# Optimization experiments

Measured on AMD Instinct MI355X. Metric: run time of the kernel, lower is better.

Reference implementation:

```python
import jax, jax.numpy as jnp
import numpy as np
import math

B, T, N, D = 8, 12, 500, 512  # batch, time(heads), nodes, K*d
FACTOR = 5
SAMPLE_K = min(FACTOR * math.ceil(math.log(N)), N)  # = 35, also n_top (N_Q == N_K)
W_SCALE = 0.02


def setup_inputs() -> dict:
    key = jax.random.key(0)
    ks = jax.random.split(key, 9)
    f32 = jnp.float32
    return {
        "X":   jax.random.normal(ks[0], (B, T, N, D), f32),
        "STE": jax.random.normal(ks[1], (B, T, N, D), f32),
        "Wq":  jax.random.normal(ks[2], (2 * D, D), f32) * W_SCALE,
        "bq":  jnp.zeros((D,), f32),
        "Wk":  jax.random.normal(ks[3], (2 * D, D), f32) * W_SCALE,
        "bk":  jnp.zeros((D,), f32),
        "Wv":  jax.random.normal(ks[4], (2 * D, D), f32) * W_SCALE,
        "bv":  jnp.zeros((D,), f32),
        "sample_idx": jax.random.randint(ks[5], (N, SAMPLE_K), 0, N, jnp.int32),
    }


def reference(X, STE, Wq, bq, Wk, bk, Wv, bv, sample_idx):
    # concat spatial features with spatio-temporal embedding -> projections
    Xc = jnp.concatenate([X, STE], axis=-1)                  # [B,T,N,2D]
    q = jax.nn.relu(Xc @ Wq + bq)                            # [B,T,N,D]
    k = jax.nn.relu(Xc @ Wk + bk)
    v = jax.nn.relu(Xc @ Wv + bv)

    n_top = SAMPLE_K
    # _prob_QK: sampled Q-K scores. Since SAMPLE_K*D >> N, computing the full
    # [B,T,N,N] score matrix and gathering the sampled columns is strictly
    # cheaper in memory than materializing K_sample [B,T,N,S,D] as torch does;
    # the math (Q_K_sample values) is identical.
    scores_full = jnp.einsum('bhld,bhmd->bhlm', q, k)        # [B,T,N,N]
    QK_sample = jnp.take_along_axis(
        scores_full, sample_idx[None, None, :, :], axis=3)   # [B,T,N,S]
    # sparsity measure M = max - mean (mean over L_K = N)
    M = QK_sample.max(axis=-1) - QK_sample.sum(axis=-1) / N  # [B,T,N]
    _, idx = jax.lax.top_k(M, n_top)                         # [B,T,n_top]

    # reduced-query full attention scores (gather rows of full scores == Q_reduce @ K^T)
    scores = jnp.take_along_axis(scores_full, idx[..., None], axis=2)  # [B,T,u,N]
    scores = scores * (1.0 / math.sqrt(D))

    # ProbMask (mask_flag=True): causal mask per selected query position
    j = jnp.arange(N)
    mask = j[None, None, None, :] > idx[..., None]           # [B,T,u,N]
    scores = jnp.where(mask, -jnp.inf, scores)
    attn = jax.nn.softmax(scores, axis=-1)                   # [B,T,u,N]
    ctx_new = jnp.einsum('bhun,bhnd->bhud', attn, v)         # [B,T,u,D]

    # initial context = causal cumsum of V, then scatter-update selected queries
    context = jnp.cumsum(v, axis=2)                          # [B,T,N,D]
    bi = jnp.arange(B)[:, None, None]
    hi = jnp.arange(T)[None, :, None]
    context = context.at[bi, hi, idx].set(ctx_new)
    # .transpose(2,1) in torch -> swap axes 1 and 2
    return context.transpose(0, 2, 1, 3)                     # [B,N,T,D]
```

## Files before the change

### kernel.cpp

```cpp
#include <hip/hip_runtime.h>
#include <math.h>

#define B_    8
#define T_    12
#define BT    96
#define NN    500
#define DD    512
#define KK    1024
#define SK    35
#define MROWS 48000

typedef __bf16 bf16x8 __attribute__((ext_vector_type(8)));
typedef float f32x4 __attribute__((ext_vector_type(4)));
typedef unsigned short u16;
typedef u16 ushort8_t __attribute__((ext_vector_type(8)));
typedef u16 ushort4_t __attribute__((ext_vector_type(4)));

__device__ __forceinline__ u16 bf_hi(float x) {
  __bf16 h = (__bf16)x;
  return __builtin_bit_cast(u16, h);
}
__device__ __forceinline__ float bf_tof(u16 b) {
  unsigned int u = ((unsigned int)b) << 16;
  return __builtin_bit_cast(float, u);
}

__global__ __launch_bounds__(256) void convW_kernel(
    const float* __restrict__ W, u16* __restrict__ Bth, u16* __restrict__ Btl)
{
  const int n = blockIdx.x;
  const int k0 = threadIdx.x * 4;
  float xs[4];
#pragma unroll
  for (int j = 0; j < 4; ++j) xs[j] = W[(size_t)(k0 + j) * 512 + n];
  ushort4_t hi, lo;
#pragma unroll
  for (int j = 0; j < 4; ++j) {
    u16 h = bf_hi(xs[j]);
    hi[j] = h;
    lo[j] = bf_hi(xs[j] - bf_tof(h));
  }
  *(ushort4_t*)(Bth + (size_t)n * 1024 + k0) = hi;
  *(ushort4_t*)(Btl + (size_t)n * 1024 + k0) = lo;
}

template<int PASSES>
__global__ __launch_bounds__(256) void mfma_proj(
    const float* __restrict__ X, const float* __restrict__ STE,
    const u16* __restrict__ Bth, const u16* __restrict__ Btl,
    const float* __restrict__ bias, float* __restrict__ out)
{
  constexpr int NT = (PASSES == 3) ? 4 : 2;
  __shared__ u16 ldsbuf[NT * 4096];
  u16* lAh = ldsbuf;
  u16* lBh = ldsbuf + 4096;
  u16* lAl = ldsbuf + ((NT == 4) ? 8192 : 0);
  u16* lBl = ldsbuf + ((NT == 4) ? 12288 : 0);
  const int tid = threadIdx.x;
  const int lane = tid & 63;
  const int wid = tid >> 6;
  const int wm = wid >> 1, wn = wid & 1;
  const int orig = blockIdx.x;
  const int xcd = orig & 7, pos = orig >> 3;
  const int wg = (xcd < 4 ? xcd * 188 : 752 + (xcd - 4) * 187) + pos;
  const int r0 = (wg >> 2) * 128;
  const int c0 = (wg & 3) * 128;
  const int fr = lane & 15, fk = lane >> 4;

  f32x4 acc[4][4];
#pragma unroll
  for (int m = 0; m < 4; ++m)
#pragma unroll
    for (int n = 0; n < 4; ++n) acc[m][n] = f32x4{0.f, 0.f, 0.f, 0.f};

  for (int kt = 0; kt < 32; ++kt) {
    const int kk0 = kt * 32;
#pragma unroll
    for (int p = 0; p < 2; ++p) {
      const int c = tid + p * 256;
      const int row = c >> 2, kc = c & 3;
      const int dst = row * 32 + ((kc ^ (row & 3)) * 8);
      const int col = kk0 + kc * 8;
      const float* src = (col < 512)
          ? (X + (size_t)(r0 + row) * 512 + col)
          : (STE + (size_t)(r0 + row) * 512 + (col - 512));
      float4 x0 = *(const float4*)src;
      float4 x1 = *(const float4*)(src + 4);
      float xs[8] = {x0.x, x0.y, x0.z, x0.w, x1.x, x1.y, x1.z, x1.w};
      ushort8_t hi, lo;
#pragma unroll
      for (int j = 0; j < 8; ++j) {
        u16 h = bf_hi(xs[j]);
        hi[j] = h;
        if (PASSES == 3) lo[j] = bf_hi(xs[j] - bf_tof(h));
      }
      *(ushort8_t*)&lAh[dst] = hi;
      if (PASSES == 3) *(ushort8_t*)&lAl[dst] = lo;
      const size_t gb = (size_t)(c0 + row) * 1024 + kk0 + kc * 8;
      *(ushort8_t*)&lBh[dst] = *(const ushort8_t*)(Bth + gb);
      if (PASSES == 3) *(ushort8_t*)&lBl[dst] = *(const ushort8_t*)(Btl + gb);
    }
    __syncthreads();
    bf16x8 ah[4], al[4], bh[4], bl[4];
#pragma unroll
    for (int m = 0; m < 4; ++m) {
      const int row = wm * 64 + m * 16 + fr;
      const int off = row * 32 + ((fk ^ (row & 3)) * 8);
      ah[m] = *(const bf16x8*)&lAh[off];
      if (PASSES == 3) al[m] = *(const bf16x8*)&lAl[off];
    }
#pragma unroll
    for (int n = 0; n < 4; ++n) {
      const int row = wn * 64 + n * 16 + fr;
      const int off = row * 32 + ((fk ^ (row & 3)) * 8);
      bh[n] = *(const bf16x8*)&lBh[off];
      if (PASSES == 3) bl[n] = *(const bf16x8*)&lBl[off];
    }
#pragma unroll
    for (int m = 0; m < 4; ++m)
#pragma unroll
      for (int n = 0; n < 4; ++n) {
        acc[m][n] = __builtin_amdgcn_mfma_f32_16x16x32_bf16(
            ah[m], bh[n], acc[m][n], 0, 0, 0);
        if (PASSES == 3) {
          acc[m][n] = __builtin_amdgcn_mfma_f32_16x16x32_bf16(
              ah[m], bl[n], acc[m][n], 0, 0, 0);
          acc[m][n] = __builtin_amdgcn_mfma_f32_16x16x32_bf16(
              al[m], bh[n], acc[m][n], 0, 0, 0);
        }
      }
    __syncthreads();
  }
#pragma unroll
  for (int n = 0; n < 4; ++n) {
    const int col = c0 + wn * 64 + n * 16 + fr;
    const float bb = bias[col];
#pragma unroll
    for (int m = 0; m < 4; ++m) {
      const int rowb = r0 + wm * 64 + m * 16 + fk * 4;
#pragma unroll
      for (int r = 0; r < 4; ++r)
        out[(size_t)(rowb + r) * 512 + col] = fmaxf(acc[m][n][r] + bb, 0.f);
    }
  }
}

__global__ __launch_bounds__(256) void sampled_M_kernel(
    const float* __restrict__ q, const float* __restrict__ k,
    const int* __restrict__ sidx, float* __restrict__ Mout)
{
  const int tid = threadIdx.x;
  const int lane = tid & 63, wid = tid >> 6;
  const int bid = blockIdx.x;
  const int xcd = bid & 7, j = bid >> 3;
  const int btg = j / 125, ub = j - btg * 125;
  const int bt = btg * 8 + xcd;
  const int nn = ub * 4 + wid;
  const int n = bt * NN + nn;
  const float* qrow = q + (size_t)n * DD + lane * 8;
  float4 q0 = *(const float4*)qrow;
  float4 q1 = *(const float4*)(qrow + 4);
  const float* kbase = k + (size_t)bt * NN * DD;
  float mx = -INFINITY, sm = 0.f;
  for (int s = 0; s < SK; ++s) {
    int m = sidx[nn * SK + s];
    const float* krow = kbase + (size_t)m * DD + lane * 8;
    float4 k0 = *(const float4*)krow;
    float4 k1 = *(const float4*)(krow + 4);
    float ss = q0.x*k0.x + q0.y*k0.y + q0.z*k0.z + q0.w*k0.w
             + q1.x*k1.x + q1.y*k1.y + q1.z*k1.z + q1.w*k1.w;
#pragma unroll
    for (int off = 32; off > 0; off >>= 1) ss += __shfl_xor(ss, off);
    mx = fmaxf(mx, ss);
    sm += ss;
  }
  if (lane == 0) Mout[n] = mx - sm * (1.0f / (float)NN);
}

__global__ __launch_bounds__(256) void topk_kernel(
    const float* __restrict__ Mb, int* __restrict__ idxb,
    int* __restrict__ sqi, int* __restrict__ su)
{
  const int bt = blockIdx.x;
  const int tid = threadIdx.x;
  __shared__ float mv[NN];
  __shared__ float rv[256];
  __shared__ int ri[256];
  __shared__ int qsel[SK];
  for (int n = tid; n < NN; n += 256) mv[n] = Mb[(size_t)bt * NN + n];
  __syncthreads();
  for (int it = 0; it < SK; ++it) {
    float bv = -INFINITY; int bi = NN;
    for (int n = tid; n < NN; n += 256) {
      float x = mv[n];
      if (x > bv) { bv = x; bi = n; }
    }
    rv[tid] = bv; ri[tid] = bi;
    __syncthreads();
    for (int sft = 128; sft > 0; sft >>= 1) {
      if (tid < sft) {
        float xv = rv[tid + sft]; int xi = ri[tid + sft];
        if (xv > rv[tid] || (xv == rv[tid] && xi < ri[tid])) {
          rv[tid] = xv; ri[tid] = xi;
        }
      }
      __syncthreads();
    }
    if (tid == 0) {
      idxb[bt * SK + it] = ri[0];
      qsel[it] = ri[0];
      mv[ri[0]] = -INFINITY;
    }
    __syncthreads();
  }
  if (tid < SK) {
    int myqi = qsel[tid];
    int rank = 0;
    for (int j = 0; j < SK; ++j) rank += (qsel[j] < myqi);
    sqi[bt * SK + rank] = myqi;
    su[bt * SK + rank] = tid;
  }
}

__global__ __launch_bounds__(256) void attn_grp_kernel(
    const float* __restrict__ q, const float* __restrict__ k,
    const float* __restrict__ v, const int* __restrict__ sqi,
    const int* __restrict__ su, float* __restrict__ ctxn)
{
  const int bid = blockIdx.x;
  const int xcd = bid & 7, j = bid >> 3;
  const int btg = j / 7, g = j - btg * 7;
  const int bt = btg * 8 + xcd;
  const int base = bt * SK + g * 5;
  const int tid = threadIdx.x;
  const int lane = tid & 63, wid = tid >> 6;

  __shared__ float sc[5][512];
  __shared__ int qg[5], ug[5];
  __shared__ float linv[5];
  if (tid < 5) { qg[tid] = sqi[base + tid]; ug[tid] = su[base + tid]; }
  __syncthreads();

  float4 qr[5][2];
#pragma unroll
  for (int jj = 0; jj < 5; ++jj) {
    const float* qp = q + ((size_t)bt * NN + qg[jj]) * DD + lane * 8;
    qr[jj][0] = *(const float4*)qp;
    qr[jj][1] = *(const float4*)(qp + 4);
  }
  const int gq = qg[4];
  const float scale = 0.044194173824159216f;

  for (int m = wid; m <= gq; m += 4) {
    const float* krow = k + ((size_t)bt * NN + m) * DD + lane * 8;
    float4 k0 = *(const float4*)krow;
    float4 k1 = *(const float4*)(krow + 4);
    float p[5];
#pragma unroll
    for (int jj = 0; jj < 5; ++jj) {
      p[jj] = qr[jj][0].x*k0.x + qr[jj][0].y*k0.y
            + qr[jj][0].z*k0.z + qr[jj][0].w*k0.w
            + qr[jj][1].x*k1.x + qr[jj][1].y*k1.y
            + qr[jj][1].z*k1.z + qr[jj][1].w*k1.w;
    }
#pragma unroll
    for (int off = 32; off > 0; off >>= 1)
#pragma unroll
      for (int jj = 0; jj < 5; ++jj) p[jj] += __shfl_xor(p[jj], off);
    if (lane == 0) {
#pragma unroll
      for (int jj = 0; jj < 5; ++jj) sc[jj][m] = p[jj] * scale;
    }
  }
  __syncthreads();

  for (int jj = wid; jj < 5; jj += 4) {
    const int qi = qg[jj];
    float mx = -INFINITY;
    for (int m = lane; m <= qi; m += 64) mx = fmaxf(mx, sc[jj][m]);
#pragma unroll
    for (int off = 32; off > 0; off >>= 1) mx = fmaxf(mx, __shfl_xor(mx, off));
    float sm = 0.f;
    for (int m = lane; m <= qi; m += 64) {
      float e = __expf(sc[jj][m] - mx);
      sc[jj][m] = e;
      sm += e;
    }
#pragma unroll
    for (int off = 32; off > 0; off >>= 1) sm += __shfl_xor(sm, off);
    if (lane == 0) linv[jj] = 1.f / sm;
  }
  __syncthreads();

  float a0[5] = {0.f,0.f,0.f,0.f,0.f}, a1[5] = {0.f,0.f,0.f,0.f,0.f};
  const float* vb = v + (size_t)bt * NN * DD;
  for (int m = 0; m <= gq; ++m) {
    float v0 = vb[(size_t)m * DD + tid];
    float v1 = vb[(size_t)m * DD + tid + 256];
#pragma unroll
    for (int jj = 0; jj < 5; ++jj) {
      if (m <= qg[jj]) {
        float w = sc[jj][m];
        a0[jj] = fmaf(w, v0, a0[jj]);
        a1[jj] = fmaf(w, v1, a1[jj]);
      }
    }
  }
#pragma unroll
  for (int jj = 0; jj < 5; ++jj) {
    const float inv = linv[jj];
    const size_t ob = ((size_t)bt * SK + ug[jj]) * DD;
    ctxn[ob + tid] = a0[jj] * inv;
    ctxn[ob + tid + 256] = a1[jj] * inv;
  }
}

__global__ __launch_bounds__(512) void vchunk_sum_kernel(
    const float* __restrict__ v, float* __restrict__ csum)
{
  const int ch = blockIdx.x, bt = blockIdx.y;
  const int d = threadIdx.x;
  const float* vb = v + ((size_t)bt * NN + ch * 50) * DD + d;
  float s = 0.f;
  for (int n = 0; n < 50; ++n) s += vb[(size_t)n * DD];
  csum[((size_t)bt * 10 + ch) * DD + d] = s;
}

__global__ __launch_bounds__(512) void cumsum_scatter2_kernel(
    const float* __restrict__ v, const int* __restrict__ idxb,
    const float* __restrict__ ctxn, const float* __restrict__ csum,
    float* __restrict__ out)
{
  const int ch = blockIdx.x, bt = blockIdx.y;
  const int b = bt / T_, t = bt % T_;
  const int d = threadIdx.x;
  const int n0 = ch * 50;
  __shared__ int sel[50];
  if (threadIdx.x < 50) sel[threadIdx.x] = -1;
  __syncthreads();
  if (threadIdx.x < SK) {
    int qi = idxb[bt * SK + threadIdx.x];
    if (qi >= n0 && qi < n0 + 50) sel[qi - n0] = threadIdx.x;
  }
  __syncthreads();
  float s = 0.f;
  for (int c = 0; c < ch; ++c) s += csum[((size_t)bt * 10 + c) * DD + d];
  for (int i = 0; i < 50; ++i) {
    s += v[((size_t)bt * NN + n0 + i) * DD + d];
    float o = s;
    int u = sel[i];
    if (u >= 0) o = ctxn[((size_t)bt * SK + u) * DD + d];
    out[(((size_t)b * NN + (n0 + i)) * T_ + t) * DD + d] = o;
  }
}

extern "C" void kernel_launch(void* const* d_in, const int* in_sizes, int n_in,
                              void* d_out, int out_size, void* d_ws, size_t ws_size,
                              hipStream_t stream) {
  const float* X   = (const float*)d_in[0];
  const float* STE = (const float*)d_in[1];
  const float* Wq  = (const float*)d_in[2];
  const float* bq  = (const float*)d_in[3];
  const float* Wk  = (const float*)d_in[4];
  const float* bk  = (const float*)d_in[5];
  const float* Wv  = (const float*)d_in[6];
  const float* bv  = (const float*)d_in[7];
  const int* sidx  = (const int*)d_in[8];
  float* out = (float*)d_out;

  float* q    = (float*)d_ws;
  float* k    = q + (size_t)MROWS * DD;
  float* v    = k + (size_t)MROWS * DD;
  float* Mb   = v + (size_t)MROWS * DD;
  int*   idxb = (int*)(Mb + MROWS);
  float* ctxn = (float*)(idxb + BT * SK);
  u16* Bqh = (u16*)(ctxn + (size_t)BT * SK * DD);
  u16* Bql = Bqh + (size_t)512 * 1024;
  u16* Bkh = Bql + (size_t)512 * 1024;
  u16* Bkl = Bkh + (size_t)512 * 1024;
  u16* Bvh = Bkl + (size_t)512 * 1024;
  u16* Bvl = Bvh + (size_t)512 * 1024;
  float* csum = (float*)Bqh;
  int*   sqi  = (int*)Bkh;
  int*   su   = sqi + BT * SK;
  (void)ws_size; (void)in_sizes; (void)n_in; (void)out_size;

  convW_kernel<<<512, 256, 0, stream>>>(Wq, Bqh, Bql);
  convW_kernel<<<512, 256, 0, stream>>>(Wk, Bkh, Bkl);
  convW_kernel<<<512, 256, 0, stream>>>(Wv, Bvh, Bvl);

  mfma_proj<3><<<1500, 256, 0, stream>>>(X, STE, Bqh, Bql, bq, q);
  mfma_proj<3><<<1500, 256, 0, stream>>>(X, STE, Bkh, Bkl, bk, k);
  mfma_proj<1><<<1500, 256, 0, stream>>>(X, STE, Bvh, Bvl, bv, v);

  sampled_M_kernel<<<12000, 256, 0, stream>>>(q, k, sidx, Mb);
  topk_kernel<<<BT, 256, 0, stream>>>(Mb, idxb, sqi, su);
  attn_grp_kernel<<<672, 256, 0, stream>>>(q, k, v, sqi, su, ctxn);
  dim3 g5(10, BT);
  vchunk_sum_kernel<<<g5, 512, 0, stream>>>(v, csum);
  cumsum_scatter2_kernel<<<g5, 512, 0, stream>>>(v, idxb, ctxn, csum, out);
}
```

Baseline: 1.074 ms.

## Split attention over key chunks with partial softmax and combine kernel

The grouped attention kernel now splits the key/value range into five chunks of 100 rows. Each block computes a partial max, partial sum and unnormalized output for its chunk, and a new combine kernel merges them with log-sum-exp rescaling. This raises block count from 672 to 3360 and shortens each block's serial loop over keys and values, which targets low parallelism and load imbalance from long causal ranges. The cost is an extra launch and a round trip of partial outputs, which are staged in the output buffer before it is overwritten.

```diff
diff --git a/kernel.cpp b/kernel.cpp
--- a/kernel.cpp
+++ b/kernel.cpp
@@ -222,24 +222,28 @@
   }
 }
 
-__global__ __launch_bounds__(256) void attn_grp_kernel(
+__global__ __launch_bounds__(256) void attn_part_kernel(
     const float* __restrict__ q, const float* __restrict__ k,
     const float* __restrict__ v, const int* __restrict__ sqi,
-    const int* __restrict__ su, float* __restrict__ ctxn)
+    float* __restrict__ pO, float* __restrict__ pm, float* __restrict__ pl)
 {
   const int bid = blockIdx.x;
   const int xcd = bid & 7, j = bid >> 3;
-  const int btg = j / 7, g = j - btg * 7;
+  const int btg = j / 35, rem = j - btg * 35;
+  const int g = rem / 5, c = rem % 5;
   const int bt = btg * 8 + xcd;
   const int base = bt * SK + g * 5;
+  const int c0 = c * 100;
   const int tid = threadIdx.x;
   const int lane = tid & 63, wid = tid >> 6;
 
-  __shared__ float sc[5][512];
-  __shared__ int qg[5], ug[5];
-  __shared__ float linv[5];
-  if (tid < 5) { qg[tid] = sqi[base + tid]; ug[tid] = su[base + tid]; }
-  __syncthreads();
+  __shared__ float sc[5][100];
+  __shared__ int qg[5];
+  __shared__ float pmx[5], psm[5];
+  if (tid < 5) qg[tid] = sqi[base + tid];
+  __syncthreads();
+  const int gq = qg[4];
+  const int mend = (gq < c0 + 99) ? gq : (c0 + 99);
 
   float4 qr[5][2];
 #pragma unroll
@@ -248,10 +252,9 @@
     qr[jj][0] = *(const float4*)qp;
     qr[jj][1] = *(const float4*)(qp + 4);
   }
-  const int gq = qg[4];
   const float scale = 0.044194173824159216f;
 
-  for (int m = wid; m <= gq; m += 4) {
+  for (int m = c0 + wid; m <= mend; m += 4) {
     const float* krow = k + ((size_t)bt * NN + m) * DD + lane * 8;
     float4 k0 = *(const float4*)krow;
     float4 k1 = *(const float4*)(krow + 4);
@@ -269,50 +272,96 @@
       for (int jj = 0; jj < 5; ++jj) p[jj] += __shfl_xor(p[jj], off);
     if (lane == 0) {
 #pragma unroll
-      for (int jj = 0; jj < 5; ++jj) sc[jj][m] = p[jj] * scale;
+      for (int jj = 0; jj < 5; ++jj) sc[jj][m - c0] = p[jj] * scale;
     }
   }
   __syncthreads();
 
   for (int jj = wid; jj < 5; jj += 4) {
-    const int qi = qg[jj];
-    float mx = -INFINITY;
-    for (int m = lane; m <= qi; m += 64) mx = fmaxf(mx, sc[jj][m]);
+    const int qe = (qg[jj] < c0 + 99) ? qg[jj] : (c0 + 99);
+    const int len = qe - c0 + 1;
+    float mx = -3e38f;
+    for (int i = lane; i < len; i += 64) mx = fmaxf(mx, sc[jj][i]);
 #pragma unroll
     for (int off = 32; off > 0; off >>= 1) mx = fmaxf(mx, __shfl_xor(mx, off));
     float sm = 0.f;
-    for (int m = lane; m <= qi; m += 64) {
-      float e = __expf(sc[jj][m] - mx);
-      sc[jj][m] = e;
+    for (int i = lane; i < len; i += 64) {
+      float e = __expf(sc[jj][i] - mx);
+      sc[jj][i] = e;
       sm += e;
     }
 #pragma unroll
     for (int off = 32; off > 0; off >>= 1) sm += __shfl_xor(sm, off);
-    if (lane == 0) linv[jj] = 1.f / sm;
+    if (lane == 0) { pmx[jj] = mx; psm[jj] = sm; }
   }
   __syncthreads();
 
   float a0[5] = {0.f,0.f,0.f,0.f,0.f}, a1[5] = {0.f,0.f,0.f,0.f,0.f};
   const float* vb = v + (size_t)bt * NN * DD;
-  for (int m = 0; m <= gq; ++m) {
+  for (int m = c0; m <= mend; ++m) {
     float v0 = vb[(size_t)m * DD + tid];
     float v1 = vb[(size_t)m * DD + tid + 256];
 #pragma unroll
     for (int jj = 0; jj < 5; ++jj) {
       if (m <= qg[jj]) {
-        float w = sc[jj][m];
+        float w = sc[jj][m - c0];
         a0[jj] = fmaf(w, v0, a0[jj]);
         a1[jj] = fmaf(w, v1, a1[jj]);
       }
     }
   }
+
+  const int pidx = (bt * 7 + g) * 5 + c;
+  if (tid < 5) {
+    pm[pidx * 5 + tid] = pmx[tid];
+    pl[pidx * 5 + tid] = psm[tid];
+  }
 #pragma unroll
   for (int jj = 0; jj < 5; ++jj) {
-    const float inv = linv[jj];
-    const size_t ob = ((size_t)bt * SK + ug[jj]) * DD;
-    ctxn[ob + tid] = a0[jj] * inv;
-    ctxn[ob + tid + 256] = a1[jj] * inv;
-  }
+    float* po = pO + ((size_t)(pidx * 5 + jj)) * DD;
+    po[tid] = a0[jj];
+    po[tid + 256] = a1[jj];
+  }
+}
+
+__global__ __launch_bounds__(512) void attn_combine_kernel(
+    const float* __restrict__ pO, const float* __restrict__ pm,
+    const float* __restrict__ pl, const int* __restrict__ su,
+    float* __restrict__ ctxn)
+{
+  const int bid = blockIdx.x;
+  const int bt = bid / SK, s = bid % SK;
+  const int g = s / 5, jj = s % 5;
+  const int d = threadIdx.x;
+  __shared__ float w[5];
+  __shared__ float linv;
+  if (d == 0) {
+    float m_[5], l_[5], mx = -3e38f;
+#pragma unroll
+    for (int c = 0; c < 5; ++c) {
+      const int pidx = (bt * 7 + g) * 5 + c;
+      m_[c] = pm[pidx * 5 + jj];
+      l_[c] = pl[pidx * 5 + jj];
+      mx = fmaxf(mx, m_[c]);
+    }
+    float lt = 0.f;
+#pragma unroll
+    for (int c = 0; c < 5; ++c) {
+      float wc = __expf(m_[c] - mx);
+      w[c] = wc;
+      lt += wc * l_[c];
+    }
+    linv = 1.f / lt;
+  }
+  __syncthreads();
+  float o = 0.f;
+#pragma unroll
+  for (int c = 0; c < 5; ++c) {
+    const int pidx = (bt * 7 + g) * 5 + c;
+    o = fmaf(w[c], pO[((size_t)(pidx * 5 + jj)) * DD + d], o);
+  }
+  const int u = su[bt * SK + s];
+  ctxn[((size_t)bt * SK + u) * DD + d] = o * linv;
 }
 
 __global__ __launch_bounds__(512) void vchunk_sum_kernel(
@@ -383,6 +432,9 @@
   float* csum = (float*)Bqh;
   int*   sqi  = (int*)Bkh;
   int*   su   = sqi + BT * SK;
+  float* pm   = (float*)(su + BT * SK);
+  float* pl   = pm + 3360 * 5;
+  float* pO   = (float*)d_out;
   (void)ws_size; (void)in_sizes; (void)n_in; (void)out_size;
 
   convW_kernel<<<512, 256, 0, stream>>>(Wq, Bqh, Bql);
@@ -395,7 +447,8 @@
 
   sampled_M_kernel<<<12000, 256, 0, stream>>>(q, k, sidx, Mb);
   topk_kernel<<<BT, 256, 0, stream>>>(Mb, idxb, sqi, su);
-  attn_grp_kernel<<<672, 256, 0, stream>>>(q, k, v, sqi, su, ctxn);
+  attn_part_kernel<<<3360, 256, 0, stream>>>(q, k, v, sqi, pO, pm, pl);
+  attn_combine_kernel<<<3360, 512, 0, stream>>>(pO, pm, pl, su, ctxn);
   dim3 g5(10, BT);
   vchunk_sum_kernel<<<g5, 512, 0, stream>>>(v, csum);
   cumsum_scatter2_kernel<<<g5, 512, 0, stream>>>(v, idxb, ctxn, csum, out);
```

Result: faster. 915.0 us (-14.8%).
